# Kernel optimization log

Measured on AMD Instinct MI355X. Metric: run time of the kernel, lower is better.

## Reference

```python
import jax, jax.numpy as jnp
import numpy as np

N = 50000      # nodes
E = 800000     # edges (avg degree 16)
IN_DIM = 256
HID_DIM = 256
OUT_DIM = 64


def _init_linear(key, d_in, d_out):
    # torch nn.Linear default init: U(-1/sqrt(fan_in), 1/sqrt(fan_in))
    s = 1.0 / np.sqrt(d_in)
    kw, kb = jax.random.split(key)
    W = jax.random.uniform(kw, (d_in, d_out), jnp.float32, -s, s)
    b = jax.random.uniform(kb, (d_out,), jnp.float32, -s, s)
    return W, b


def setup_inputs() -> dict:
    key = jax.random.key(0)
    ks = jax.random.split(key, 8)
    x = jax.random.normal(ks[0], (N, IN_DIM), dtype=jnp.float32)
    edge_index = jax.random.randint(ks[1], (2, E), 0, N, dtype=jnp.int64)
    dims = [(IN_DIM, HID_DIM), (HID_DIM, HID_DIM), (HID_DIM, OUT_DIM)]
    out = {"x": x, "edge_index": edge_index}
    for i, (di, do) in enumerate(dims):
        Wl, b = _init_linear(ks[2 + 2 * i], di, do)      # lin_l (on aggregated), with bias
        s = 1.0 / np.sqrt(di)
        Wr = jax.random.uniform(ks[3 + 2 * i], (di, do), jnp.float32, -s, s)  # lin_r (root), no bias
        out[f"Wl{i}"] = Wl
        out[f"Wr{i}"] = Wr
        out[f"b{i}"] = b
    return out


def sage_conv(x, src, dst, Wl, Wr, b):
    # PyG SAGEConv with mean aggregation:
    # out = lin_l(mean_{j in N(i)} x_j) + lin_r(x_i)
    n = x.shape[0]
    msg = x[src]                                              # [E, d] gather
    agg_sum = jax.ops.segment_sum(msg, dst, num_segments=n)   # [N, d] scatter-add
    deg = jax.ops.segment_sum(jnp.ones((src.shape[0], 1), x.dtype), dst, num_segments=n)
    agg = agg_sum / jnp.maximum(deg, 1.0)                     # mean, safe for isolated nodes
    return agg @ Wl + x @ Wr + b


def reference(x, edge_index, Wl0, Wr0, b0, Wl1, Wr1, b1, Wl2, Wr2, b2):
    src, dst = edge_index[0], edge_index[1]
    # dropout is identity in eval mode
    h = jax.nn.relu(sage_conv(x, src, dst, Wl0, Wr0, b0))
    h = jax.nn.relu(sage_conv(h, src, dst, Wl1, Wr1, b1))
    return sage_conv(h, src, dst, Wl2, Wr2, b2)
```

## Files before the change

kernel.cpp:

```cpp
#include <hip/hip_runtime.h>


typedef short bf16x8 __attribute__((ext_vector_type(8)));
typedef float f32x4 __attribute__((ext_vector_type(4)));

__device__ __forceinline__ unsigned short f2bf(float f) {
    unsigned int b = __float_as_uint(f);
    b += 0x7fffu + ((b >> 16) & 1u);
    return (unsigned short)(b >> 16);
}
__device__ __forceinline__ float bflo(unsigned int u) { return __uint_as_float(u << 16); }
__device__ __forceinline__ float bfhi(unsigned int u) { return __uint_as_float(u & 0xffff0000u); }

__device__ __forceinline__ void gload_lds16(const void* g, void* l) {
    __builtin_amdgcn_global_load_lds(
        (const __attribute__((address_space(1))) void*)g,
        (__attribute__((address_space(3))) void*)l, 16, 0, 0);
}

__global__ void fillpos_prep_kernel(
        const int* __restrict__ ei, int* __restrict__ cursor, int* __restrict__ pos,
        int E, int nPosBlk,
        const float* __restrict__ x, unsigned short* __restrict__ xb,
        const float* __restrict__ Wl0, const float* __restrict__ Wr0,
        unsigned short* __restrict__ BT0,
        const float* __restrict__ Wl1, const float* __restrict__ Wr1,
        unsigned short* __restrict__ BT1,
        const float* __restrict__ Wl2, unsigned short* __restrict__ BT2l,
        const float* __restrict__ Wr2, unsigned short* __restrict__ BT2r,
        int n4) {
    if (blockIdx.x < nPosBlk) {
        int e = blockIdx.x * 256 + threadIdx.x;
        if (e < E) pos[e] = atomicAdd(&cursor[ei[E + e]], 1);
        return;
    }
    int t = (blockIdx.x - nPosBlk) * 256 + threadIdx.x;
    if (t < n4) {
        float4 v = ((const float4*)x)[t];
        ushort4 o;
        o.x = f2bf(v.x); o.y = f2bf(v.y); o.z = f2bf(v.z); o.w = f2bf(v.w);
        ((ushort4*)xb)[t] = o;
        return;
    }
    t -= n4;
    if (t < 131072) {
        int k = t >> 8, n = t & 255;
        float v = (k < 256) ? Wl0[(size_t)k * 256 + n] : Wr0[(size_t)(k - 256) * 256 + n];
        BT0[(size_t)n * 512 + k] = f2bf(v);
        return;
    }
    t -= 131072;
    if (t < 131072) {
        int k = t >> 8, n = t & 255;
        float v = (k < 256) ? Wl1[(size_t)k * 256 + n] : Wr1[(size_t)(k - 256) * 256 + n];
        BT1[(size_t)n * 512 + k] = f2bf(v);
        return;
    }
    t -= 131072;
    if (t < 16384) {
        int k = t >> 6, n = t & 63;
        BT2l[(size_t)n * 256 + k] = f2bf(Wl2[(size_t)k * 64 + n]);
        return;
    }
    t -= 16384;
    if (t < 16384) {
        int k = t >> 6, n = t & 63;
        BT2r[(size_t)n * 256 + k] = f2bf(Wr2[(size_t)k * 64 + n]);
    }
}

__global__ __launch_bounds__(1024) void scan1_kernel(
        const int* __restrict__ deg, int* __restrict__ incl, int* __restrict__ bsum, int n) {
    __shared__ int wsum[16];
    __shared__ int woff[16];
    const int tid = threadIdx.x, lane = tid & 63, wid = tid >> 6;
    int i = blockIdx.x * 1024 + tid;
    int x = (i < n) ? deg[i] : 0;
    #pragma unroll
    for (int off = 1; off < 64; off <<= 1) {
        int t = __shfl_up(x, off, 64);
        if (lane >= off) x += t;
    }
    if (lane == 63) wsum[wid] = x;
    __syncthreads();
    if (tid == 0) {
        int s = 0;
        #pragma unroll
        for (int w = 0; w < 16; ++w) { woff[w] = s; s += wsum[w]; }
        bsum[blockIdx.x] = s;
    }
    __syncthreads();
    if (i < n) incl[i] = x + woff[wid];
}

__global__ void scan3_kernel(const int* __restrict__ incl, const int* __restrict__ bsum,
                             int* __restrict__ row_ptr, int n, int nb) {
    __shared__ int off_s;
    const int chunk = blockIdx.x >> 2;
    if (threadIdx.x < 64) {
        int lane = threadIdx.x;
        int v = (lane < chunk && lane < nb) ? bsum[lane] : 0;
        #pragma unroll
        for (int m = 1; m < 64; m <<= 1) v += __shfl_xor(v, m, 64);
        if (lane == 0) off_s = v;
    }
    __syncthreads();
    int i = blockIdx.x * 256 + threadIdx.x;
    if (i == 0) row_ptr[0] = 0;
    if (i < n) row_ptr[i + 1] = incl[i] + off_s;
}

__global__ void fill_scatter_kernel(const int* __restrict__ ei, const int* __restrict__ pos,
                                    const int* __restrict__ row_ptr, int* __restrict__ col, int E) {
    int e = blockIdx.x * blockDim.x + threadIdx.x;
    if (e < E) {
        int d = ei[E + e];
        col[row_ptr[d] + pos[e]] = ei[e];
    }
}

__global__ __launch_bounds__(256) void aggregate256_kernel(
        const unsigned short* __restrict__ h, const int* __restrict__ row_ptr,
        const int* __restrict__ col, unsigned short* __restrict__ agg, int n) {
    int node = blockIdx.x * 4 + (threadIdx.x >> 6);
    int lane = threadIdx.x & 63;
    if (node >= n) return;
    const int start = row_ptr[node], end = row_ptr[node + 1];
    const int half = lane >> 5;
    const int fo = (lane & 31) * 8;
    float a[8] = {0.f, 0.f, 0.f, 0.f, 0.f, 0.f, 0.f, 0.f};
    int eb = start;
    for (; eb + 4 <= end; eb += 4) {
        int e0 = eb + half, e1 = eb + 2 + half;
        uint4 v0 = *(const uint4*)(h + (size_t)col[e0] * 256 + fo);
        uint4 v1 = *(const uint4*)(h + (size_t)col[e1] * 256 + fo);
        a[0] += bflo(v0.x) + bflo(v1.x); a[1] += bfhi(v0.x) + bfhi(v1.x);
        a[2] += bflo(v0.y) + bflo(v1.y); a[3] += bfhi(v0.y) + bfhi(v1.y);
        a[4] += bflo(v0.z) + bflo(v1.z); a[5] += bfhi(v0.z) + bfhi(v1.z);
        a[6] += bflo(v0.w) + bflo(v1.w); a[7] += bfhi(v0.w) + bfhi(v1.w);
    }
    for (; eb < end; eb += 2) {
        int e = eb + half;
        if (e < end) {
            uint4 v = *(const uint4*)(h + (size_t)col[e] * 256 + fo);
            a[0] += bflo(v.x); a[1] += bfhi(v.x);
            a[2] += bflo(v.y); a[3] += bfhi(v.y);
            a[4] += bflo(v.z); a[5] += bfhi(v.z);
            a[6] += bflo(v.w); a[7] += bfhi(v.w);
        }
    }
    #pragma unroll
    for (int i = 0; i < 8; ++i) a[i] += __shfl_xor(a[i], 32, 64);
    int d = end - start;
    float inv = 1.0f / (float)(d > 1 ? d : 1);
    if (lane < 32) {
        ushort4 o0, o1;
        o0.x = f2bf(a[0] * inv); o0.y = f2bf(a[1] * inv);
        o0.z = f2bf(a[2] * inv); o0.w = f2bf(a[3] * inv);
        o1.x = f2bf(a[4] * inv); o1.y = f2bf(a[5] * inv);
        o1.z = f2bf(a[6] * inv); o1.w = f2bf(a[7] * inv);
        *(ushort4*)(agg + (size_t)node * 256 + fo) = o0;
        *(ushort4*)(agg + (size_t)node * 256 + fo + 4) = o1;
    }
}

__global__ __launch_bounds__(256) void agg64_add_kernel(
        const unsigned short* __restrict__ p, const int* __restrict__ row_ptr,
        const int* __restrict__ col, float* __restrict__ out, int n) {
    int node = blockIdx.x * 4 + (threadIdx.x >> 6);
    int lane = threadIdx.x & 63;
    if (node >= n) return;
    const int start = row_ptr[node], end = row_ptr[node + 1];
    const int g = lane >> 4;
    const int fo = (lane & 15) * 4;
    float a0 = 0.f, a1 = 0.f, a2 = 0.f, a3 = 0.f;
    int eb = start;
    for (; eb + 8 <= end; eb += 8) {
        int e0 = eb + g, e1 = eb + 4 + g;
        uint2 v0 = *(const uint2*)(p + (size_t)col[e0] * 64 + fo);
        uint2 v1 = *(const uint2*)(p + (size_t)col[e1] * 64 + fo);
        a0 += bflo(v0.x) + bflo(v1.x); a1 += bfhi(v0.x) + bfhi(v1.x);
        a2 += bflo(v0.y) + bflo(v1.y); a3 += bfhi(v0.y) + bfhi(v1.y);
    }
    for (; eb < end; eb += 4) {
        int e = eb + g;
        if (e < end) {
            uint2 v = *(const uint2*)(p + (size_t)col[e] * 64 + fo);
            a0 += bflo(v.x); a1 += bfhi(v.x);
            a2 += bflo(v.y); a3 += bfhi(v.y);
        }
    }
    #pragma unroll
    for (int m = 16; m <= 32; m <<= 1) {
        a0 += __shfl_xor(a0, m, 64);
        a1 += __shfl_xor(a1, m, 64);
        a2 += __shfl_xor(a2, m, 64);
        a3 += __shfl_xor(a3, m, 64);
    }
    int d = end - start;
    float inv = 1.0f / (float)(d > 1 ? d : 1);
    if (lane < 16) {
        float* dst = out + (size_t)node * 64 + fo;
        float4 base = *(float4*)dst;
        float4 o = make_float4(base.x + a0 * inv, base.y + a1 * inv,
                               base.z + a2 * inv, base.w + a3 * inv);
        *(float4*)dst = o;
    }
}

template<int NKS, int NT, bool RELU>
__global__ __launch_bounds__(256, 2) void gemm_mfma_kernel(
        const unsigned short* __restrict__ A0, const unsigned short* __restrict__ A1,
        const unsigned short* __restrict__ BT, const float* __restrict__ bias,
        unsigned short* __restrict__ Cout, int M, int Nc) {
    constexpr int BN = NT * 32;
    constexpr int KB = NKS * 32;
    __shared__ unsigned short As[128 * 32];
    __shared__ unsigned short Bs[BN * 32];
    const int tid = threadIdx.x;
    const int lane = tid & 63;
    const int wid = tid >> 6;
    const int wr = wid >> 1, wc = wid & 1;
    const int row0 = blockIdx.x * 128;
    const int col0 = blockIdx.y * BN;

    f32x4 acc[4][NT];
    #pragma unroll
    for (int i = 0; i < 4; ++i)
        #pragma unroll
        for (int j = 0; j < NT; ++j) acc[i][j] = (f32x4){0.f, 0.f, 0.f, 0.f};

    const int rA = tid >> 2;
    const int kc = (tid & 3) * 8;

    for (int ks = 0; ks < NKS; ++ks) {
        const unsigned short* Asrc = (ks < 8) ? A0 : A1;
        const int ka = (ks & 7) * 32;
        #pragma unroll
        for (int i = 0; i < 2; ++i) {
            const unsigned short* g = Asrc + (size_t)(row0 + rA + i * 64) * 256 + ka + kc;
            gload_lds16(g, As + (size_t)i * 2048 + tid * 8);
        }
        #pragma unroll
        for (int i = 0; i < NT / 2; ++i) {
            const unsigned short* g = BT + (size_t)(col0 + rA + i * 64) * KB + ks * 32 + kc;
            gload_lds16(g, Bs + (size_t)i * 2048 + tid * 8);
        }
        __syncthreads();

        bf16x8 a[4], b[NT];
        #pragma unroll
        for (int tm = 0; tm < 4; ++tm)
            a[tm] = *(const bf16x8*)&As[(wr * 64 + tm * 16 + (lane & 15)) * 32 + (lane >> 4) * 8];
        #pragma unroll
        for (int tn = 0; tn < NT; ++tn)
            b[tn] = *(const bf16x8*)&Bs[(wc * NT * 16 + tn * 16 + (lane & 15)) * 32 + (lane >> 4) * 8];
        #pragma unroll
        for (int tm = 0; tm < 4; ++tm)
            #pragma unroll
            for (int tn = 0; tn < NT; ++tn)
                acc[tm][tn] = __builtin_amdgcn_mfma_f32_16x16x32_bf16(a[tm], b[tn], acc[tm][tn], 0, 0, 0);
        __syncthreads();
    }

    const int cb = col0 + wc * NT * 16;
    #pragma unroll
    for (int tn = 0; tn < NT; ++tn) {
        int colg = cb + tn * 16 + (lane & 15);
        float bv = bias[colg];
        #pragma unroll
        for (int tm = 0; tm < 4; ++tm) {
            #pragma unroll
            for (int r = 0; r < 4; ++r) {
                int row = row0 + wr * 64 + tm * 16 + (lane >> 4) * 4 + r;
                if (row < M) {
                    float v = acc[tm][tn][r] + bv;
                    if (RELU) v = fmaxf(v, 0.f);
                    Cout[(size_t)row * Nc + colg] = f2bf(v);
                }
            }
        }
    }
}

__global__ __launch_bounds__(256, 2) void gemm2_dual_kernel(
        const unsigned short* __restrict__ A,
        const unsigned short* __restrict__ BTl,
        const unsigned short* __restrict__ BTr,
        const float* __restrict__ bias,
        unsigned short* __restrict__ P2,
        float* __restrict__ Out, int M) {
    __shared__ unsigned short As[128 * 32];
    __shared__ unsigned short Bl[64 * 32];
    __shared__ unsigned short Br[64 * 32];
    const int tid = threadIdx.x;
    const int lane = tid & 63;
    const int wid = tid >> 6;
    const int wr = wid >> 1, wc = wid & 1;
    const int row0 = blockIdx.x * 128;

    f32x4 accL[4][2], accR[4][2];
    #pragma unroll
    for (int i = 0; i < 4; ++i)
        #pragma unroll
        for (int j = 0; j < 2; ++j) {
            accL[i][j] = (f32x4){0.f, 0.f, 0.f, 0.f};
            accR[i][j] = (f32x4){0.f, 0.f, 0.f, 0.f};
        }

    const int rA = tid >> 2;
    const int kc = (tid & 3) * 8;

    for (int ks = 0; ks < 8; ++ks) {
        const int ka = ks * 32;
        #pragma unroll
        for (int i = 0; i < 2; ++i) {
            const unsigned short* g = A + (size_t)(row0 + rA + i * 64) * 256 + ka + kc;
            gload_lds16(g, As + (size_t)i * 2048 + tid * 8);
        }
        gload_lds16(BTl + (size_t)rA * 256 + ka + kc, Bl + tid * 8);
        gload_lds16(BTr + (size_t)rA * 256 + ka + kc, Br + tid * 8);
        __syncthreads();

        bf16x8 a[4], bl[2], br[2];
        #pragma unroll
        for (int tm = 0; tm < 4; ++tm)
            a[tm] = *(const bf16x8*)&As[(wr * 64 + tm * 16 + (lane & 15)) * 32 + (lane >> 4) * 8];
        #pragma unroll
        for (int tn = 0; tn < 2; ++tn) {
            int bi = (wc * 32 + tn * 16 + (lane & 15)) * 32 + (lane >> 4) * 8;
            bl[tn] = *(const bf16x8*)&Bl[bi];
            br[tn] = *(const bf16x8*)&Br[bi];
        }
        #pragma unroll
        for (int tm = 0; tm < 4; ++tm)
            #pragma unroll
            for (int tn = 0; tn < 2; ++tn) {
                accL[tm][tn] = __builtin_amdgcn_mfma_f32_16x16x32_bf16(a[tm], bl[tn], accL[tm][tn], 0, 0, 0);
                accR[tm][tn] = __builtin_amdgcn_mfma_f32_16x16x32_bf16(a[tm], br[tn], accR[tm][tn], 0, 0, 0);
            }
        __syncthreads();
    }

    #pragma unroll
    for (int tn = 0; tn < 2; ++tn) {
        int colg = wc * 32 + tn * 16 + (lane & 15);
        float bv = bias[colg];
        #pragma unroll
        for (int tm = 0; tm < 4; ++tm) {
            #pragma unroll
            for (int r = 0; r < 4; ++r) {
                int row = row0 + wr * 64 + tm * 16 + (lane >> 4) * 4 + r;
                if (row < M) {
                    P2[(size_t)row * 64 + colg] = f2bf(accL[tm][tn][r]);
                    Out[(size_t)row * 64 + colg] = accR[tm][tn][r] + bv;
                }
            }
        }
    }
}

extern "C" void kernel_launch(void* const* d_in, const int* in_sizes, int n_in,
                              void* d_out, int out_size, void* d_ws, size_t ws_size,
                              hipStream_t stream) {
    const float* x   = (const float*)d_in[0];
    const int*   ei  = (const int*)d_in[1];
    const float* Wl0 = (const float*)d_in[2];
    const float* Wr0 = (const float*)d_in[3];
    const float* b0  = (const float*)d_in[4];
    const float* Wl1 = (const float*)d_in[5];
    const float* Wr1 = (const float*)d_in[6];
    const float* b1  = (const float*)d_in[7];
    const float* Wl2 = (const float*)d_in[8];
    const float* Wr2 = (const float*)d_in[9];
    const float* b2  = (const float*)d_in[10];
    float* out = (float*)d_out;

    const int Nn = in_sizes[0] / 256;
    const int E  = in_sizes[1] / 2;
    const int Mpad = ((Nn + 127) / 128) * 128;
    const int nb = (Nn + 1023) / 1024;

    char* ws = (char*)d_ws;
    size_t off = 0;
    auto take = [&](size_t bytes) -> void* {
        void* p = (void*)(ws + off);
        off += (bytes + 255) & ~(size_t)255;
        return p;
    };
    int* cursor  = (int*)take((size_t)Nn * 4);
    int* incl    = (int*)take((size_t)Nn * 4);
    int* bsum    = (int*)take((size_t)64 * 4);
    int* row_ptr = (int*)take((size_t)(Nn + 1) * 4);
    int* col     = (int*)take((size_t)E * 4);
    int* pos     = (int*)take((size_t)E * 4);
    unsigned short* xb  = (unsigned short*)take((size_t)Mpad * 256 * 2);
    unsigned short* h1  = (unsigned short*)take((size_t)Mpad * 256 * 2);
    unsigned short* h2  = (unsigned short*)take((size_t)Mpad * 256 * 2);
    unsigned short* h3  = (unsigned short*)take((size_t)Mpad * 256 * 2);
    unsigned short* p2  = (unsigned short*)take((size_t)Mpad * 64 * 2);
    unsigned short* BT0  = (unsigned short*)take((size_t)256 * 512 * 2);
    unsigned short* BT1  = (unsigned short*)take((size_t)256 * 512 * 2);
    unsigned short* BT2l = (unsigned short*)take((size_t)64 * 256 * 2);
    unsigned short* BT2r = (unsigned short*)take((size_t)64 * 256 * 2);
    (void)ws_size; (void)n_in; (void)out_size;

    hipMemsetAsync(cursor, 0, (size_t)Nn * 4, stream);
    const int n4 = Nn * 64;
    const int nPosBlk = (E + 255) / 256;
    const int prepTot = n4 + 131072 + 131072 + 16384 + 16384;
    const int nPrepBlk = (prepTot + 255) / 256;
    fillpos_prep_kernel<<<nPosBlk + nPrepBlk, 256, 0, stream>>>(
        ei, cursor, pos, E, nPosBlk,
        x, xb, Wl0, Wr0, BT0, Wl1, Wr1, BT1, Wl2, BT2l, Wr2, BT2r, n4);
    scan1_kernel<<<nb, 1024, 0, stream>>>(cursor, incl, bsum, Nn);
    scan3_kernel<<<(Nn + 255) / 256, 256, 0, stream>>>(incl, bsum, row_ptr, Nn, nb);
    fill_scatter_kernel<<<(E + 255) / 256, 256, 0, stream>>>(ei, pos, row_ptr, col, E);

    const int gx = Mpad / 128;
    const int aggGrid = (Nn + 3) / 4;

    aggregate256_kernel<<<aggGrid, 256, 0, stream>>>(xb, row_ptr, col, h1, Nn);
    gemm_mfma_kernel<16, 8, true><<<dim3(gx, 1), 256, 0, stream>>>(
        h1, xb, BT0, b0, h2, Nn, 256);
    aggregate256_kernel<<<aggGrid, 256, 0, stream>>>(h2, row_ptr, col, h1, Nn);
    gemm_mfma_kernel<16, 8, true><<<dim3(gx, 1), 256, 0, stream>>>(
        h1, h2, BT1, b1, h3, Nn, 256);
    gemm2_dual_kernel<<<gx, 256, 0, stream>>>(h3, BT2l, BT2r, b2, p2, out, Nn);
    agg64_add_kernel<<<aggGrid, 256, 0, stream>>>(p2, row_ptr, col, out, Nn);
}
```

Baseline: 296.5 us.

## Split layer GEMM into root and neighbor halves, overlap root GEMM with aggregation

Each of the first two layers used to run an aggregation kernel and then one GEMM over the concatenated [agg | x] input. Now the root-term GEMM (x @ Wr + b) runs in the same launch as the gather-aggregation, in separate blocks, so the compute-bound MFMA work can overlap the memory-bound gather. A second GEMM then computes agg @ Wl, adds the stored bf16 root result and applies ReLU. The change adds an extra bf16 intermediate buffer write and read, rounds the root partial sum to bf16, and gives the aggregation blocks the GEMM's shared-memory footprint and launch bounds, which may lower their occupancy.

```diff
diff --git a/kernel.cpp b/kernel.cpp
--- a/kernel.cpp
+++ b/kernel.cpp
@@ -11,6 +11,7 @@
 }
 __device__ __forceinline__ float bflo(unsigned int u) { return __uint_as_float(u << 16); }
 __device__ __forceinline__ float bfhi(unsigned int u) { return __uint_as_float(u & 0xffff0000u); }
+__device__ __forceinline__ float bf2f(unsigned short u) { return __uint_as_float((unsigned)u << 16); }
 
 __device__ __forceinline__ void gload_lds16(const void* g, void* l) {
     __builtin_amdgcn_global_load_lds(
@@ -22,10 +23,10 @@
         const int* __restrict__ ei, int* __restrict__ cursor, int* __restrict__ pos,
         int E, int nPosBlk,
         const float* __restrict__ x, unsigned short* __restrict__ xb,
-        const float* __restrict__ Wl0, const float* __restrict__ Wr0,
-        unsigned short* __restrict__ BT0,
-        const float* __restrict__ Wl1, const float* __restrict__ Wr1,
-        unsigned short* __restrict__ BT1,
+        const float* __restrict__ Wl0, unsigned short* __restrict__ BT0l,
+        const float* __restrict__ Wr0, unsigned short* __restrict__ BT0r,
+        const float* __restrict__ Wl1, unsigned short* __restrict__ BT1l,
+        const float* __restrict__ Wr1, unsigned short* __restrict__ BT1r,
         const float* __restrict__ Wl2, unsigned short* __restrict__ BT2l,
         const float* __restrict__ Wr2, unsigned short* __restrict__ BT2r,
         int n4) {
@@ -43,30 +44,17 @@
         return;
     }
     t -= n4;
-    if (t < 131072) {
-        int k = t >> 8, n = t & 255;
-        float v = (k < 256) ? Wl0[(size_t)k * 256 + n] : Wr0[(size_t)(k - 256) * 256 + n];
-        BT0[(size_t)n * 512 + k] = f2bf(v);
-        return;
-    }
-    t -= 131072;
-    if (t < 131072) {
-        int k = t >> 8, n = t & 255;
-        float v = (k < 256) ? Wl1[(size_t)k * 256 + n] : Wr1[(size_t)(k - 256) * 256 + n];
-        BT1[(size_t)n * 512 + k] = f2bf(v);
-        return;
-    }
-    t -= 131072;
-    if (t < 16384) {
-        int k = t >> 6, n = t & 63;
-        BT2l[(size_t)n * 256 + k] = f2bf(Wl2[(size_t)k * 64 + n]);
-        return;
-    }
+    if (t < 65536) { int k = t >> 8, n = t & 255; BT0l[(size_t)n * 256 + k] = f2bf(Wl0[(size_t)k * 256 + n]); return; }
+    t -= 65536;
+    if (t < 65536) { int k = t >> 8, n = t & 255; BT0r[(size_t)n * 256 + k] = f2bf(Wr0[(size_t)k * 256 + n]); return; }
+    t -= 65536;
+    if (t < 65536) { int k = t >> 8, n = t & 255; BT1l[(size_t)n * 256 + k] = f2bf(Wl1[(size_t)k * 256 + n]); return; }
+    t -= 65536;
+    if (t < 65536) { int k = t >> 8, n = t & 255; BT1r[(size_t)n * 256 + k] = f2bf(Wr1[(size_t)k * 256 + n]); return; }
+    t -= 65536;
+    if (t < 16384) { int k = t >> 6, n = t & 63; BT2l[(size_t)n * 256 + k] = f2bf(Wl2[(size_t)k * 64 + n]); return; }
     t -= 16384;
-    if (t < 16384) {
-        int k = t >> 6, n = t & 63;
-        BT2r[(size_t)n * 256 + k] = f2bf(Wr2[(size_t)k * 64 + n]);
-    }
+    if (t < 16384) { int k = t >> 6, n = t & 63; BT2r[(size_t)n * 256 + k] = f2bf(Wr2[(size_t)k * 64 + n]); }
 }
 
 __global__ __launch_bounds__(1024) void scan1_kernel(
@@ -119,48 +107,176 @@
     }
 }
 
-__global__ __launch_bounds__(256) void aggregate256_kernel(
-        const unsigned short* __restrict__ h, const int* __restrict__ row_ptr,
-        const int* __restrict__ col, unsigned short* __restrict__ agg, int n) {
-    int node = blockIdx.x * 4 + (threadIdx.x >> 6);
-    int lane = threadIdx.x & 63;
-    if (node >= n) return;
-    const int start = row_ptr[node], end = row_ptr[node + 1];
-    const int half = lane >> 5;
-    const int fo = (lane & 31) * 8;
-    float a[8] = {0.f, 0.f, 0.f, 0.f, 0.f, 0.f, 0.f, 0.f};
-    int eb = start;
-    for (; eb + 4 <= end; eb += 4) {
-        int e0 = eb + half, e1 = eb + 2 + half;
-        uint4 v0 = *(const uint4*)(h + (size_t)col[e0] * 256 + fo);
-        uint4 v1 = *(const uint4*)(h + (size_t)col[e1] * 256 + fo);
-        a[0] += bflo(v0.x) + bflo(v1.x); a[1] += bfhi(v0.x) + bfhi(v1.x);
-        a[2] += bflo(v0.y) + bflo(v1.y); a[3] += bfhi(v0.y) + bfhi(v1.y);
-        a[4] += bflo(v0.z) + bflo(v1.z); a[5] += bfhi(v0.z) + bfhi(v1.z);
-        a[6] += bflo(v0.w) + bflo(v1.w); a[7] += bfhi(v0.w) + bfhi(v1.w);
-    }
-    for (; eb < end; eb += 2) {
-        int e = eb + half;
-        if (e < end) {
-            uint4 v = *(const uint4*)(h + (size_t)col[e] * 256 + fo);
-            a[0] += bflo(v.x); a[1] += bfhi(v.x);
-            a[2] += bflo(v.y); a[3] += bfhi(v.y);
-            a[4] += bflo(v.z); a[5] += bfhi(v.z);
-            a[6] += bflo(v.w); a[7] += bfhi(v.w);
-        }
-    }
-    #pragma unroll
-    for (int i = 0; i < 8; ++i) a[i] += __shfl_xor(a[i], 32, 64);
-    int d = end - start;
-    float inv = 1.0f / (float)(d > 1 ? d : 1);
-    if (lane < 32) {
-        ushort4 o0, o1;
-        o0.x = f2bf(a[0] * inv); o0.y = f2bf(a[1] * inv);
-        o0.z = f2bf(a[2] * inv); o0.w = f2bf(a[3] * inv);
-        o1.x = f2bf(a[4] * inv); o1.y = f2bf(a[5] * inv);
-        o1.z = f2bf(a[6] * inv); o1.w = f2bf(a[7] * inv);
-        *(ushort4*)(agg + (size_t)node * 256 + fo) = o0;
-        *(ushort4*)(agg + (size_t)node * 256 + fo + 4) = o1;
+__global__ __launch_bounds__(256, 2) void agg_gemmR_kernel(
+        const unsigned short* __restrict__ hsrc, const int* __restrict__ row_ptr,
+        const int* __restrict__ col, unsigned short* __restrict__ aggdst,
+        const unsigned short* __restrict__ BTr, const float* __restrict__ bias,
+        unsigned short* __restrict__ r, int n, int aggGrid, int M) {
+    __shared__ unsigned short As[128 * 32];
+    __shared__ unsigned short Bs[256 * 32];
+
+    if (blockIdx.x < aggGrid) {
+        int node = blockIdx.x * 4 + (threadIdx.x >> 6);
+        int lane = threadIdx.x & 63;
+        if (node >= n) return;
+        const int start = row_ptr[node], end = row_ptr[node + 1];
+        const int half = lane >> 5;
+        const int fo = (lane & 31) * 8;
+        float a[8] = {0.f, 0.f, 0.f, 0.f, 0.f, 0.f, 0.f, 0.f};
+        int eb = start;
+        for (; eb + 4 <= end; eb += 4) {
+            int e0 = eb + half, e1 = eb + 2 + half;
+            uint4 v0 = *(const uint4*)(hsrc + (size_t)col[e0] * 256 + fo);
+            uint4 v1 = *(const uint4*)(hsrc + (size_t)col[e1] * 256 + fo);
+            a[0] += bflo(v0.x) + bflo(v1.x); a[1] += bfhi(v0.x) + bfhi(v1.x);
+            a[2] += bflo(v0.y) + bflo(v1.y); a[3] += bfhi(v0.y) + bfhi(v1.y);
+            a[4] += bflo(v0.z) + bflo(v1.z); a[5] += bfhi(v0.z) + bfhi(v1.z);
+            a[6] += bflo(v0.w) + bflo(v1.w); a[7] += bfhi(v0.w) + bfhi(v1.w);
+        }
+        for (; eb < end; eb += 2) {
+            int e = eb + half;
+            if (e < end) {
+                uint4 v = *(const uint4*)(hsrc + (size_t)col[e] * 256 + fo);
+                a[0] += bflo(v.x); a[1] += bfhi(v.x);
+                a[2] += bflo(v.y); a[3] += bfhi(v.y);
+                a[4] += bflo(v.z); a[5] += bfhi(v.z);
+                a[6] += bflo(v.w); a[7] += bfhi(v.w);
+            }
+        }
+        #pragma unroll
+        for (int i = 0; i < 8; ++i) a[i] += __shfl_xor(a[i], 32, 64);
+        int d = end - start;
+        float inv = 1.0f / (float)(d > 1 ? d : 1);
+        if (lane < 32) {
+            ushort4 o0, o1;
+            o0.x = f2bf(a[0] * inv); o0.y = f2bf(a[1] * inv);
+            o0.z = f2bf(a[2] * inv); o0.w = f2bf(a[3] * inv);
+            o1.x = f2bf(a[4] * inv); o1.y = f2bf(a[5] * inv);
+            o1.z = f2bf(a[6] * inv); o1.w = f2bf(a[7] * inv);
+            *(ushort4*)(aggdst + (size_t)node * 256 + fo) = o0;
+            *(ushort4*)(aggdst + (size_t)node * 256 + fo + 4) = o1;
+        }
+        return;
+    }
+
+    const int tid = threadIdx.x;
+    const int lane = tid & 63;
+    const int wid = tid >> 6;
+    const int wr = wid >> 1, wc = wid & 1;
+    const int row0 = (blockIdx.x - aggGrid) * 128;
+
+    f32x4 acc[4][8];
+    #pragma unroll
+    for (int i = 0; i < 4; ++i)
+        #pragma unroll
+        for (int j = 0; j < 8; ++j) acc[i][j] = (f32x4){0.f, 0.f, 0.f, 0.f};
+
+    const int rA = tid >> 2;
+    const int kc = (tid & 3) * 8;
+
+    for (int ks = 0; ks < 8; ++ks) {
+        const int ka = ks * 32;
+        #pragma unroll
+        for (int i = 0; i < 2; ++i)
+            gload_lds16(hsrc + (size_t)(row0 + rA + i * 64) * 256 + ka + kc,
+                        As + (size_t)i * 2048 + tid * 8);
+        #pragma unroll
+        for (int i = 0; i < 4; ++i)
+            gload_lds16(BTr + (size_t)(rA + i * 64) * 256 + ka + kc,
+                        Bs + (size_t)i * 2048 + tid * 8);
+        __syncthreads();
+
+        bf16x8 a[4], b[8];
+        #pragma unroll
+        for (int tm = 0; tm < 4; ++tm)
+            a[tm] = *(const bf16x8*)&As[(wr * 64 + tm * 16 + (lane & 15)) * 32 + (lane >> 4) * 8];
+        #pragma unroll
+        for (int tn = 0; tn < 8; ++tn)
+            b[tn] = *(const bf16x8*)&Bs[(wc * 128 + tn * 16 + (lane & 15)) * 32 + (lane >> 4) * 8];
+        #pragma unroll
+        for (int tm = 0; tm < 4; ++tm)
+            #pragma unroll
+            for (int tn = 0; tn < 8; ++tn)
+                acc[tm][tn] = __builtin_amdgcn_mfma_f32_16x16x32_bf16(a[tm], b[tn], acc[tm][tn], 0, 0, 0);
+        __syncthreads();
+    }
+
+    #pragma unroll
+    for (int tn = 0; tn < 8; ++tn) {
+        int colg = wc * 128 + tn * 16 + (lane & 15);
+        float bv = bias[colg];
+        #pragma unroll
+        for (int tm = 0; tm < 4; ++tm) {
+            #pragma unroll
+            for (int rr = 0; rr < 4; ++rr) {
+                int row = row0 + wr * 64 + tm * 16 + (lane >> 4) * 4 + rr;
+                if (row < M) r[(size_t)row * 256 + colg] = f2bf(acc[tm][tn][rr] + bv);
+            }
+        }
+    }
+}
+
+__global__ __launch_bounds__(256, 2) void gemmL_kernel(
+        const unsigned short* __restrict__ Agg, const unsigned short* __restrict__ BTl,
+        const unsigned short* __restrict__ r, unsigned short* __restrict__ Cout, int M) {
+    __shared__ unsigned short As[128 * 32];
+    __shared__ unsigned short Bs[256 * 32];
+    const int tid = threadIdx.x;
+    const int lane = tid & 63;
+    const int wid = tid >> 6;
+    const int wr = wid >> 1, wc = wid & 1;
+    const int row0 = blockIdx.x * 128;
+
+    f32x4 acc[4][8];
+    #pragma unroll
+    for (int i = 0; i < 4; ++i)
+        #pragma unroll
+        for (int j = 0; j < 8; ++j) acc[i][j] = (f32x4){0.f, 0.f, 0.f, 0.f};
+
+    const int rA = tid >> 2;
+    const int kc = (tid & 3) * 8;
+
+    for (int ks = 0; ks < 8; ++ks) {
+        const int ka = ks * 32;
+        #pragma unroll
+        for (int i = 0; i < 2; ++i)
+            gload_lds16(Agg + (size_t)(row0 + rA + i * 64) * 256 + ka + kc,
+                        As + (size_t)i * 2048 + tid * 8);
+        #pragma unroll
+        for (int i = 0; i < 4; ++i)
+            gload_lds16(BTl + (size_t)(rA + i * 64) * 256 + ka + kc,
+                        Bs + (size_t)i * 2048 + tid * 8);
+        __syncthreads();
+
+        bf16x8 a[4], b[8];
+        #pragma unroll
+        for (int tm = 0; tm < 4; ++tm)
+            a[tm] = *(const bf16x8*)&As[(wr * 64 + tm * 16 + (lane & 15)) * 32 + (lane >> 4) * 8];
+        #pragma unroll
+        for (int tn = 0; tn < 8; ++tn)
+            b[tn] = *(const bf16x8*)&Bs[(wc * 128 + tn * 16 + (lane & 15)) * 32 + (lane >> 4) * 8];
+        #pragma unroll
+        for (int tm = 0; tm < 4; ++tm)
+            #pragma unroll
+            for (int tn = 0; tn < 8; ++tn)
+                acc[tm][tn] = __builtin_amdgcn_mfma_f32_16x16x32_bf16(a[tm], b[tn], acc[tm][tn], 0, 0, 0);
+        __syncthreads();
+    }
+
+    #pragma unroll
+    for (int tn = 0; tn < 8; ++tn) {
+        int colg = wc * 128 + tn * 16 + (lane & 15);
+        #pragma unroll
+        for (int tm = 0; tm < 4; ++tm) {
+            #pragma unroll
+            for (int rr = 0; rr < 4; ++rr) {
+                int row = row0 + wr * 64 + tm * 16 + (lane >> 4) * 4 + rr;
+                if (row < M) {
+                    float v = acc[tm][tn][rr] + bf2f(r[(size_t)row * 256 + colg]);
+                    Cout[(size_t)row * 256 + colg] = f2bf(fmaxf(v, 0.f));
+                }
+            }
+        }
     }
 }
 
@@ -208,81 +324,6 @@
     }
 }
 
-template<int NKS, int NT, bool RELU>
-__global__ __launch_bounds__(256, 2) void gemm_mfma_kernel(
-        const unsigned short* __restrict__ A0, const unsigned short* __restrict__ A1,
-        const unsigned short* __restrict__ BT, const float* __restrict__ bias,
-        unsigned short* __restrict__ Cout, int M, int Nc) {
-    constexpr int BN = NT * 32;
-    constexpr int KB = NKS * 32;
-    __shared__ unsigned short As[128 * 32];
-    __shared__ unsigned short Bs[BN * 32];
-    const int tid = threadIdx.x;
-    const int lane = tid & 63;
-    const int wid = tid >> 6;
-    const int wr = wid >> 1, wc = wid & 1;
-    const int row0 = blockIdx.x * 128;
-    const int col0 = blockIdx.y * BN;
-
-    f32x4 acc[4][NT];
-    #pragma unroll
-    for (int i = 0; i < 4; ++i)
-        #pragma unroll
-        for (int j = 0; j < NT; ++j) acc[i][j] = (f32x4){0.f, 0.f, 0.f, 0.f};
-
-    const int rA = tid >> 2;
-    const int kc = (tid & 3) * 8;
-
-    for (int ks = 0; ks < NKS; ++ks) {
-        const unsigned short* Asrc = (ks < 8) ? A0 : A1;
-        const int ka = (ks & 7) * 32;
-        #pragma unroll
-        for (int i = 0; i < 2; ++i) {
-            const unsigned short* g = Asrc + (size_t)(row0 + rA + i * 64) * 256 + ka + kc;
-            gload_lds16(g, As + (size_t)i * 2048 + tid * 8);
-        }
-        #pragma unroll
-        for (int i = 0; i < NT / 2; ++i) {
-            const unsigned short* g = BT + (size_t)(col0 + rA + i * 64) * KB + ks * 32 + kc;
-            gload_lds16(g, Bs + (size_t)i * 2048 + tid * 8);
-        }
-        __syncthreads();
-
-        bf16x8 a[4], b[NT];
-        #pragma unroll
-        for (int tm = 0; tm < 4; ++tm)
-            a[tm] = *(const bf16x8*)&As[(wr * 64 + tm * 16 + (lane & 15)) * 32 + (lane >> 4) * 8];
-        #pragma unroll
-        for (int tn = 0; tn < NT; ++tn)
-            b[tn] = *(const bf16x8*)&Bs[(wc * NT * 16 + tn * 16 + (lane & 15)) * 32 + (lane >> 4) * 8];
-        #pragma unroll
-        for (int tm = 0; tm < 4; ++tm)
-            #pragma unroll
-            for (int tn = 0; tn < NT; ++tn)
-                acc[tm][tn] = __builtin_amdgcn_mfma_f32_16x16x32_bf16(a[tm], b[tn], acc[tm][tn], 0, 0, 0);
-        __syncthreads();
-    }
-
-    const int cb = col0 + wc * NT * 16;
-    #pragma unroll
-    for (int tn = 0; tn < NT; ++tn) {
-        int colg = cb + tn * 16 + (lane & 15);
-        float bv = bias[colg];
-        #pragma unroll
-        for (int tm = 0; tm < 4; ++tm) {
-            #pragma unroll
-            for (int r = 0; r < 4; ++r) {
-                int row = row0 + wr * 64 + tm * 16 + (lane >> 4) * 4 + r;
-                if (row < M) {
-                    float v = acc[tm][tn][r] + bv;
-                    if (RELU) v = fmaxf(v, 0.f);
-                    Cout[(size_t)row * Nc + colg] = f2bf(v);
-                }
-            }
-        }
-    }
-}
-
 __global__ __launch_bounds__(256, 2) void gemm2_dual_kernel(
         const unsigned short* __restrict__ A,
         const unsigned short* __restrict__ BTl,
@@ -349,11 +390,11 @@
         #pragma unroll
         for (int tm = 0; tm < 4; ++tm) {
             #pragma unroll
-            for (int r = 0; r < 4; ++r) {
-                int row = row0 + wr * 64 + tm * 16 + (lane >> 4) * 4 + r;
+            for (int rr = 0; rr < 4; ++rr) {
+                int row = row0 + wr * 64 + tm * 16 + (lane >> 4) * 4 + rr;
                 if (row < M) {
-                    P2[(size_t)row * 64 + colg] = f2bf(accL[tm][tn][r]);
-                    Out[(size_t)row * 64 + colg] = accR[tm][tn][r] + bv;
+                    P2[(size_t)row * 64 + colg] = f2bf(accL[tm][tn][rr]);
+                    Out[(size_t)row * 64 + colg] = accR[tm][tn][rr] + bv;
                 }
             }
         }
@@ -398,9 +439,12 @@
     unsigned short* h1  = (unsigned short*)take((size_t)Mpad * 256 * 2);
     unsigned short* h2  = (unsigned short*)take((size_t)Mpad * 256 * 2);
     unsigned short* h3  = (unsigned short*)take((size_t)Mpad * 256 * 2);
+    unsigned short* rbuf = (unsigned short*)take((size_t)Mpad * 256 * 2);
     unsigned short* p2  = (unsigned short*)take((size_t)Mpad * 64 * 2);
-    unsigned short* BT0  = (unsigned short*)take((size_t)256 * 512 * 2);
-    unsigned short* BT1  = (unsigned short*)take((size_t)256 * 512 * 2);
+    unsigned short* BT0l = (unsigned short*)take((size_t)256 * 256 * 2);
+    unsigned short* BT0r = (unsigned short*)take((size_t)256 * 256 * 2);
+    unsigned short* BT1l = (unsigned short*)take((size_t)256 * 256 * 2);
+    unsigned short* BT1r = (unsigned short*)take((size_t)256 * 256 * 2);
     unsigned short* BT2l = (unsigned short*)take((size_t)64 * 256 * 2);
     unsigned short* BT2r = (unsigned short*)take((size_t)64 * 256 * 2);
     (void)ws_size; (void)n_in; (void)out_size;
@@ -408,11 +452,11 @@
     hipMemsetAsync(cursor, 0, (size_t)Nn * 4, stream);
     const int n4 = Nn * 64;
     const int nPosBlk = (E + 255) / 256;
-    const int prepTot = n4 + 131072 + 131072 + 16384 + 16384;
+    const int prepTot = n4 + 4 * 65536 + 2 * 16384;
     const int nPrepBlk = (prepTot + 255) / 256;
     fillpos_prep_kernel<<<nPosBlk + nPrepBlk, 256, 0, stream>>>(
         ei, cursor, pos, E, nPosBlk,
-        x, xb, Wl0, Wr0, BT0, Wl1, Wr1, BT1, Wl2, BT2l, Wr2, BT2r, n4);
+        x, xb, Wl0, BT0l, Wr0, BT0r, Wl1, BT1l, Wr1, BT1r, Wl2, BT2l, Wr2, BT2r, n4);
     scan1_kernel<<<nb, 1024, 0, stream>>>(cursor, incl, bsum, Nn);
     scan3_kernel<<<(Nn + 255) / 256, 256, 0, stream>>>(incl, bsum, row_ptr, Nn, nb);
     fill_scatter_kernel<<<(E + 255) / 256, 256, 0, stream>>>(ei, pos, row_ptr, col, E);
@@ -420,12 +464,12 @@
     const int gx = Mpad / 128;
     const int aggGrid = (Nn + 3) / 4;
 
-    aggregate256_kernel<<<aggGrid, 256, 0, stream>>>(xb, row_ptr, col, h1, Nn);
-    gemm_mfma_kernel<16, 8, true><<<dim3(gx, 1), 256, 0, stream>>>(
-        h1, xb, BT0, b0, h2, Nn, 256);
-    aggregate256_kernel<<<aggGrid, 256, 0, stream>>>(h2, row_ptr, col, h1, Nn);
-    gemm_mfma_kernel<16, 8, true><<<dim3(gx, 1), 256, 0, stream>>>(
-        h1, h2, BT1, b1, h3, Nn, 256);
+    agg_gemmR_kernel<<<aggGrid + gx, 256, 0, stream>>>(
+        xb, row_ptr, col, h1, BT0r, b0, rbuf, Nn, aggGrid, Nn);
+    gemmL_kernel<<<gx, 256, 0, stream>>>(h1, BT0l, rbuf, h2, Nn);
+    agg_gemmR_kernel<<<aggGrid + gx, 256, 0, stream>>>(
+        h2, row_ptr, col, h1, BT1r, b1, rbuf, Nn, aggGrid, Nn);
+    gemmL_kernel<<<gx, 256, 0, stream>>>(h1, BT1l, rbuf, h3, Nn);
     gemm2_dual_kernel<<<gx, 256, 0, stream>>>(h3, BT2l, BT2r, b2, p2, out, Nn);
     agg64_add_kernel<<<aggGrid, 256, 0, stream>>>(p2, row_ptr, col, out, Nn);
 }
```

Measured after the change: 499.5 us. 1.68x slower.
